# Kernel tuning notes

Measured on AMD Instinct MI355X. Metric: run time of the kernel, lower is better.

The kernel has to match this reference:

```python
import jax, jax.numpy as jnp
import numpy as np

N_NODES = 50000
N_EDGES = 800000
DIM = 128  # in_dim == out_dim (required by the original module's math)
BN_EPS = 1e-5


def setup_inputs() -> dict:
    key = jax.random.key(0)
    ks = jax.random.split(key, 12)
    d = DIM
    s = 1.0 / np.sqrt(d)
    x = jax.random.normal(ks[0], (N_NODES, d), dtype=jnp.float32)
    edge_index = jax.random.randint(ks[1], (2, N_EDGES), 0, N_NODES, dtype=jnp.int64)
    # message_fn: Linear(in_dim, out_dim)
    W_msg = jax.random.uniform(ks[2], (d, d), jnp.float32, -s, s)
    b_msg = jax.random.uniform(ks[3], (d,), jnp.float32, -s, s)
    # attention: Linear(2*in_dim, 1)
    sa = 1.0 / np.sqrt(2 * d)
    W_att = jax.random.uniform(ks[4], (2 * d, 1), jnp.float32, -sa, sa)
    b_att = jax.random.uniform(ks[5], (1,), jnp.float32, -sa, sa)
    # GRUCell(out_dim, out_dim): weight_ih [3d, d], weight_hh [3d, d]
    W_ih = jax.random.uniform(ks[6], (3 * d, d), jnp.float32, -s, s)
    b_ih = jax.random.uniform(ks[7], (3 * d,), jnp.float32, -s, s)
    W_hh = jax.random.uniform(ks[8], (3 * d, d), jnp.float32, -s, s)
    b_hh = jax.random.uniform(ks[9], (3 * d,), jnp.float32, -s, s)
    # BatchNorm1d(out_dim)
    gamma = jnp.ones((d,), jnp.float32)
    beta = jnp.zeros((d,), jnp.float32)
    return {"x": x, "edge_index": edge_index, "W_msg": W_msg, "b_msg": b_msg,
            "W_att": W_att, "b_att": b_att, "W_ih": W_ih, "b_ih": b_ih,
            "W_hh": W_hh, "b_hh": b_hh, "gamma": gamma, "beta": beta}


def reference(x, edge_index, W_msg, b_msg, W_att, b_att, W_ih, b_ih, W_hh, b_hh, gamma, beta):
    num_nodes, d = x.shape
    src = edge_index[0]
    dst = edge_index[1]
    xs = x[src]            # [E, d] gather
    xd = x[dst]            # [E, d] gather
    # sigmoid(cat([xs, xd]) @ W_att + b_att) without materializing the concat
    att = jax.nn.sigmoid(xs @ W_att[:d] + xd @ W_att[d:] + b_att)  # [E, 1]
    messages = (xs @ W_msg + b_msg) * att                          # [E, d]
    aggregated = jax.ops.segment_sum(messages, dst, num_segments=num_nodes)  # scatter-add
    # GRUCell(aggregated, x)
    gi = aggregated @ W_ih.T + b_ih   # [N, 3d]
    gh = x @ W_hh.T + b_hh            # [N, 3d]
    i_r, i_z, i_n = jnp.split(gi, 3, axis=1)
    h_r, h_z, h_n = jnp.split(gh, 3, axis=1)
    r = jax.nn.sigmoid(i_r + h_r)
    z = jax.nn.sigmoid(i_z + h_z)
    n = jnp.tanh(i_n + r * h_n)
    h_new = (1.0 - z) * n + z * x
    # dropout is identity in eval mode; BatchNorm1d in training mode (batch stats, biased var)
    mean = jnp.mean(h_new, axis=0)
    var = jnp.var(h_new, axis=0)
    return gamma * (h_new - mean) * jax.lax.rsqrt(var + BN_EPS) + beta
```

## Files before the change

### kernel.cpp

```cpp
#include <hip/hip_runtime.h>
#include <hip/hip_bf16.h>
#include <hip/hip_fp16.h>

#define DIM 128
#define SWS 136
typedef __hip_bfloat16 bf16;
typedef __attribute__((ext_vector_type(8))) short bf16x8;
typedef __attribute__((ext_vector_type(4))) float f32x4;

__device__ __forceinline__ float b2f(bf16 v) { return __bfloat162float(v); }
__device__ __forceinline__ bf16  f2b(float v) { return __float2bfloat16(v); }

template<bool F32>
__device__ __forceinline__ float ldf(const void* p, size_t i) {
    if (F32) return ((const float*)p)[i];
    else     return b2f(((const bf16*)p)[i]);
}
template<bool F32>
__device__ __forceinline__ void stf(void* p, size_t i, float v) {
    if (F32) ((float*)p)[i] = v;
    else     ((bf16*)p)[i] = f2b(v);
}

__device__ __forceinline__ bf16x8 pack8_f32(const float* p) {
    bf16x8 r;
#pragma unroll
    for (int i = 0; i < 8; ++i) { bf16 t = f2b(p[i]); r[i] = *(const short*)&t; }
    return r;
}
template<bool F32>
__device__ __forceinline__ bf16x8 load_frag(const void* base, size_t off) {
    if (F32) return pack8_f32((const float*)base + off);
    else     return *(const bf16x8*)((const unsigned short*)base + off);
}

__device__ __forceinline__ float bflo(unsigned int m) { return __uint_as_float(m << 16); }
__device__ __forceinline__ float bfhi(unsigned int m) { return __uint_as_float(m & 0xFFFF0000u); }

__device__ __forceinline__ float sigmoidf_fast(float v) { return 1.0f / (1.0f + __expf(-v)); }
__device__ __forceinline__ float tanhf_fast(float t) {
    float e2 = __expf(2.0f * t);
    return 1.0f - 2.0f / (e2 + 1.0f);
}

__global__ void detect_kernel(const void* __restrict__ ei, const void* __restrict__ gamma,
                              int n_nodes, int* __restrict__ flags)
{
    if (blockIdx.x == 0 && threadIdx.x == 0) {
        const long long* e64 = (const long long*)ei;
        int ok = 1;
        for (int i = 0; i < 16; ++i) {
            long long v = e64[i];
            if (v < 0 || v >= (long long)n_nodes) ok = 0;
        }
        flags[0] = ok;
        const float* g = (const float*)gamma;
        flags[1] = (fabsf(g[0] - 1.0f) < 1e-6f && fabsf(g[1] - 1.0f) < 1e-6f) ? 1 : 0;
    }
}

__device__ void atomic_add_bf16(bf16* addr, float val)
{
    unsigned int* base = (unsigned int*)((size_t)addr & ~(size_t)3);
    bool hi = ((size_t)addr & 2) != 0;
    unsigned int old = *base, assumed;
    do {
        assumed = old;
        unsigned short cur = hi ? (unsigned short)(assumed >> 16) : (unsigned short)(assumed & 0xFFFF);
        bf16 cb = *(bf16*)&cur;
        bf16 nb = f2b(b2f(cb) + val);
        unsigned short ns = *(unsigned short*)&nb;
        unsigned int newv = hi ? ((assumed & 0x0000FFFFu) | ((unsigned int)ns << 16))
                               : ((assumed & 0xFFFF0000u) | (unsigned int)ns);
        old = atomicCAS(base, assumed, newv);
    } while (old != assumed);
}

#define NW (144 * 128)
#define NI (384 * 128)
#define PREPN (NW + 2 * NI)
__global__ __launch_bounds__(256) void prep_hist_kernel(
    const void* __restrict__ W_msg, const void* __restrict__ W_att,
    const void* __restrict__ W_ih, const void* __restrict__ W_hh,
    unsigned short* __restrict__ wbuf,
    const void* __restrict__ ei, int* __restrict__ deg, int n_edges,
    int prep_blocks, const int* __restrict__ flags)
{
    if ((int)blockIdx.x < prep_blocks) {
        bool f32 = flags[1] != 0;
        int i = blockIdx.x * blockDim.x + threadIdx.x;
        if (i >= PREPN) return;
        float v;
        if (i < NW) {
            int j = i >> 7, k = i & 127;
            if (j < 128)       v = f32 ? ((const float*)W_msg)[k * 128 + j] : b2f(((const bf16*)W_msg)[k * 128 + j]);
            else if (j == 128) v = f32 ? ((const float*)W_att)[k]           : b2f(((const bf16*)W_att)[k]);
            else if (j == 129) v = f32 ? ((const float*)W_att)[128 + k]     : b2f(((const bf16*)W_att)[128 + k]);
            else               v = 0.0f;
        } else if (i < NW + NI) {
            int t = i - NW;
            v = f32 ? ((const float*)W_ih)[t] : b2f(((const bf16*)W_ih)[t]);
        } else {
            int t = i - NW - NI;
            v = f32 ? ((const float*)W_hh)[t] : b2f(((const bf16*)W_hh)[t]);
        }
        bf16 b = f2b(v);
        wbuf[i] = *(unsigned short*)&b;
    } else {
        int i = ((int)blockIdx.x - prep_blocks) * blockDim.x + threadIdx.x;
        if (i >= n_edges) return;
        int t = flags[0] ? (int)((const long long*)ei)[n_edges + i] : ((const int*)ei)[n_edges + i];
        atomicAdd(&deg[t], 1);
    }
}

template<bool F32>
__device__ void node_mfma_body(unsigned short* __restrict__ sw,
                               const void* __restrict__ x, const unsigned short* __restrict__ Wnode,
                               const void* __restrict__ b_msg, unsigned short* __restrict__ Mb,
                               float* __restrict__ a_src, float* __restrict__ a_dst, int n_nodes)
{
    int wave = threadIdx.x >> 6, lane = threadIdx.x & 63;
    int m0 = (blockIdx.x * 4 + wave) * 16;
    int mrow = lane & 15, quad = lane >> 4;
    bool active = (m0 < n_nodes);
    int mnode = active ? (m0 + mrow < n_nodes ? m0 + mrow : n_nodes - 1) : 0;

    {
        int t = threadIdx.x;
#pragma unroll
        for (int i = 0; i < 9; ++i) {
            int v = t + i * 256;
            if (v < 2304) {
                int row = v >> 4, col = (v & 15) * 8;
                *(bf16x8*)(sw + row * SWS + col) = *(const bf16x8*)(Wnode + row * DIM + col);
            }
        }
    }

    bf16x8 a[4];
#pragma unroll
    for (int kq = 0; kq < 4; ++kq)
        a[kq] = load_frag<F32>(x, (size_t)mnode * DIM + kq * 32 + quad * 8);

    __syncthreads();

#pragma unroll
    for (int jt = 0; jt < 9; ++jt) {
        const unsigned short* wr = sw + (jt * 16 + mrow) * SWS + quad * 8;
        bf16x8 B[4];
#pragma unroll
        for (int kq = 0; kq < 4; ++kq)
            B[kq] = *(const bf16x8*)(wr + kq * 32);
        f32x4 acc = {0, 0, 0, 0};
#pragma unroll
        for (int kq = 0; kq < 4; ++kq)
            acc = __builtin_amdgcn_mfma_f32_16x16x32_bf16(a[kq], B[kq], acc, 0, 0, 0);
        if (!active) continue;
        if (jt < 8) {
            int jcol = jt * 16 + mrow;
            float bm = ldf<F32>(b_msg, jcol);
#pragma unroll
            for (int rg = 0; rg < 4; ++rg) {
                int node = m0 + quad * 4 + rg;
                if (node < n_nodes) {
                    bf16 bb = f2b(acc[rg] + bm);
                    Mb[(size_t)node * DIM + jcol] = *(unsigned short*)&bb;
                }
            }
        } else if (mrow < 2) {
#pragma unroll
            for (int rg = 0; rg < 4; ++rg) {
                int node = m0 + quad * 4 + rg;
                if (node < n_nodes) {
                    if (mrow == 0) a_src[node] = acc[rg];
                    else           a_dst[node] = acc[rg];
                }
            }
        }
    }
}

__global__ __launch_bounds__(256) void node_mfma_kernel(
    const void* x, const unsigned short* Wnode, const void* b_msg,
    unsigned short* Mb, float* a_src, float* a_dst, int n_nodes, const int* __restrict__ flags)
{
    __shared__ unsigned short sw[144 * SWS];
    if (flags[1]) node_mfma_body<true>(sw, x, Wnode, b_msg, Mb, a_src, a_dst, n_nodes);
    else          node_mfma_body<false>(sw, x, Wnode, b_msg, Mb, a_src, a_dst, n_nodes);
}

__global__ __launch_bounds__(256) void partial_sum_kernel(
    const int* __restrict__ deg, int* __restrict__ partials, int n_nodes)
{
    __shared__ int s[256];
    int t = threadIdx.x;
    int i = blockIdx.x * 256 + t;
    s[t] = (i < n_nodes) ? deg[i] : 0;
    __syncthreads();
    for (int off = 128; off > 0; off >>= 1) {
        if (t < off) s[t] += s[t + off];
        __syncthreads();
    }
    if (t == 0) partials[blockIdx.x] = s[0];
}

__global__ __launch_bounds__(256) void scan_write_kernel(
    const int* __restrict__ deg, const int* __restrict__ partials,
    int* __restrict__ row_start, int* __restrict__ fill, int n_nodes, int n_edges,
    int nblocks)
{
    __shared__ int s[256];
    __shared__ int sp[256];
    int t = threadIdx.x;
    int i = blockIdx.x * 256 + t;
    int v = (i < n_nodes) ? deg[i] : 0;
    int pv = (t < nblocks) ? partials[t] : 0;
    s[t] = v;
    sp[t] = pv;
    __syncthreads();
    for (int off = 1; off < 256; off <<= 1) {
        int u  = (t >= off) ? s[t - off]  : 0;
        int up = (t >= off) ? sp[t - off] : 0;
        __syncthreads();
        s[t] += u;
        sp[t] += up;
        __syncthreads();
    }
    int block_off = (blockIdx.x == 0) ? 0 : sp[blockIdx.x - 1];
    int excl = s[t] - v + block_off;
    if (i < n_nodes) { row_start[i] = excl; fill[i] = excl; }
    if (blockIdx.x == 0 && t == 0) row_start[n_nodes] = n_edges;
}

template<bool PACK4>
__global__ __launch_bounds__(256) void scatter_kernel(
    const void* __restrict__ ei, const float* __restrict__ a_src, const float* __restrict__ a_dst,
    const void* __restrict__ b_att, int* __restrict__ fill,
    void* __restrict__ edata, const int* __restrict__ flags, int n_edges)
{
    int i = blockIdx.x * blockDim.x + threadIdx.x;
    if (i >= n_edges) return;
    int s, t;
    if (flags[0]) {
        const long long* p = (const long long*)ei;
        s = (int)p[i]; t = (int)p[n_edges + i];
    } else {
        const int* p = (const int*)ei;
        s = p[i]; t = p[n_edges + i];
    }
    float battv = flags[1] ? ((const float*)b_att)[0] : b2f(((const bf16*)b_att)[0]);
    int pos = atomicAdd(&fill[t], 1);
    float logit = a_src[s] + a_dst[t] + battv;
    float att = 1.0f / (1.0f + __expf(-logit));
    if (PACK4) {
        __half h = __float2half(att);
        unsigned int rec = ((unsigned int)s << 16) | (unsigned int)(*(unsigned short*)&h);
        ((unsigned int*)edata)[pos] = rec;
    } else {
        uint2 rec;
        rec.x = (unsigned int)s;
        rec.y = __float_as_uint(att);
        ((uint2*)edata)[pos] = rec;
    }
}

template<bool PACK4>
__global__ __launch_bounds__(256) void aggregate_kernel(
    const unsigned short* __restrict__ Mb, const int* __restrict__ row_start,
    const void* __restrict__ edata, unsigned short* __restrict__ aggb, int n_nodes)
{
    int w = (int)((blockIdx.x * (unsigned)blockDim.x + threadIdx.x) >> 6);
    int lane = threadIdx.x & 63;
    if (w >= n_nodes) return;
    int beg = row_start[w], end = row_start[w + 1];
    float acc0 = 0.0f, acc1 = 0.0f;
    const unsigned int* e4 = (const unsigned int*)edata;
    const uint2* e8 = (const uint2*)edata;
    int e = beg;
    for (; e + 4 <= end; e += 4) {
        unsigned int src[4]; float wt[4];
#pragma unroll
        for (int k = 0; k < 4; ++k) {
            if (PACK4) {
                unsigned int r = e4[e + k];
                src[k] = r >> 16;
                unsigned short hb = (unsigned short)(r & 0xFFFF);
                wt[k] = __half2float(*(__half*)&hb);
            } else {
                uint2 r = e8[e + k];
                src[k] = r.x;
                wt[k] = __uint_as_float(r.y);
            }
        }
        unsigned int m0 = *(const unsigned int*)(Mb + ((size_t)src[0] << 7) + lane * 2);
        unsigned int m1 = *(const unsigned int*)(Mb + ((size_t)src[1] << 7) + lane * 2);
        unsigned int m2 = *(const unsigned int*)(Mb + ((size_t)src[2] << 7) + lane * 2);
        unsigned int m3 = *(const unsigned int*)(Mb + ((size_t)src[3] << 7) + lane * 2);
        acc0 += wt[0] * bflo(m0) + wt[1] * bflo(m1) + wt[2] * bflo(m2) + wt[3] * bflo(m3);
        acc1 += wt[0] * bfhi(m0) + wt[1] * bfhi(m1) + wt[2] * bfhi(m2) + wt[3] * bfhi(m3);
    }
    for (; e < end; ++e) {
        unsigned int sidx; float a;
        if (PACK4) {
            unsigned int r = e4[e];
            sidx = r >> 16;
            unsigned short hb = (unsigned short)(r & 0xFFFF);
            a = __half2float(*(__half*)&hb);
        } else {
            uint2 r = e8[e];
            sidx = r.x;
            a = __uint_as_float(r.y);
        }
        unsigned int m = *(const unsigned int*)(Mb + ((size_t)sidx << 7) + lane * 2);
        acc0 += a * bflo(m);
        acc1 += a * bfhi(m);
    }
    bf16 r0 = f2b(acc0), r1 = f2b(acc1);
    unsigned int packed = (unsigned int)(*(unsigned short*)&r0) |
                          ((unsigned int)(*(unsigned short*)&r1) << 16);
    *(unsigned int*)(aggb + ((size_t)w << 7) + lane * 2) = packed;
}

template<bool F32>
__device__ void gru_mfma_body(unsigned short* __restrict__ sw,
                              const void* __restrict__ x, const unsigned short* __restrict__ aggb,
                              const unsigned short* __restrict__ Wih, const unsigned short* __restrict__ Whh,
                              const void* __restrict__ b_ih, const void* __restrict__ b_hh,
                              void* __restrict__ h_out, int n_nodes)
{
    const int BUF = 96 * SWS;
    int wave = threadIdx.x >> 6, lane = threadIdx.x & 63;
    int m0 = (blockIdx.x * 4 + wave) * 16;
    int mrow = lane & 15, quad = lane >> 4;
    bool active = (m0 < n_nodes);
    int mnode = active ? (m0 + mrow < n_nodes ? m0 + mrow : n_nodes - 1) : 0;

    int t = threadIdx.x;
    int srow[6], scol[6];
    const unsigned short* sbase[6];
#pragma unroll
    for (int i = 0; i < 6; ++i) {
        int v = t + i * 256;
        int row = v >> 4;
        scol[i] = (v & 15) * 8;
        srow[i] = row;
        int g = row >> 4;
        sbase[i] = ((g < 3) ? Wih : Whh) + (size_t)((g % 3) * 128 + (row & 15)) * DIM;
    }

    bf16x8 a_ag[4], a_x[4];
#pragma unroll
    for (int kq = 0; kq < 4; ++kq) {
        a_ag[kq] = *(const bf16x8*)(aggb + (size_t)mnode * DIM + kq * 32 + quad * 8);
        a_x[kq]  = load_frag<F32>(x, (size_t)mnode * DIM + kq * 32 + quad * 8);
    }

#pragma unroll
    for (int i = 0; i < 6; ++i) {
        bf16x8 d = *(const bf16x8*)(sbase[i] + scol[i]);
        *(bf16x8*)(sw + srow[i] * SWS + scol[i]) = d;
    }
    __syncthreads();

    float hprev[4];

    for (int jt = 0; jt < 8; ++jt) {
        unsigned short* cur = sw + (jt & 1) * BUF;
        unsigned short* nxt = sw + ((jt + 1) & 1) * BUF;

        bf16x8 pf[6];
        if (jt < 7) {
#pragma unroll
            for (int i = 0; i < 6; ++i)
                pf[i] = *(const bf16x8*)(sbase[i] + (size_t)(jt + 1) * 16 * DIM + scol[i]);
        }

        f32x4 acc_ir = {0,0,0,0}, acc_iz = {0,0,0,0}, acc_in = {0,0,0,0};
        f32x4 acc_hr = {0,0,0,0}, acc_hz = {0,0,0,0}, acc_hn = {0,0,0,0};

#pragma unroll
        for (int half = 0; half < 2; ++half) {
            bf16x8 B[12];
#pragma unroll
            for (int kq = 0; kq < 2; ++kq) {
                int k = half * 2 + kq;
                int boff = mrow * SWS + k * 32 + quad * 8;
#pragma unroll
                for (int g = 0; g < 6; ++g)
                    B[kq * 6 + g] = *(const bf16x8*)(cur + g * (16 * SWS) + boff);
            }
#pragma unroll
            for (int kq = 0; kq < 2; ++kq) {
                int k = half * 2 + kq;
                acc_ir = __builtin_amdgcn_mfma_f32_16x16x32_bf16(a_ag[k], B[kq * 6 + 0], acc_ir, 0, 0, 0);
                acc_iz = __builtin_amdgcn_mfma_f32_16x16x32_bf16(a_ag[k], B[kq * 6 + 1], acc_iz, 0, 0, 0);
                acc_in = __builtin_amdgcn_mfma_f32_16x16x32_bf16(a_ag[k], B[kq * 6 + 2], acc_in, 0, 0, 0);
                acc_hr = __builtin_amdgcn_mfma_f32_16x16x32_bf16(a_x[k],  B[kq * 6 + 3], acc_hr, 0, 0, 0);
                acc_hz = __builtin_amdgcn_mfma_f32_16x16x32_bf16(a_x[k],  B[kq * 6 + 4], acc_hz, 0, 0, 0);
                acc_hn = __builtin_amdgcn_mfma_f32_16x16x32_bf16(a_x[k],  B[kq * 6 + 5], acc_hn, 0, 0, 0);
            }
        }

        if (jt < 7) {
#pragma unroll
            for (int i = 0; i < 6; ++i)
                *(bf16x8*)(nxt + srow[i] * SWS + scol[i]) = pf[i];
        }

        if (active) {
            int jcol = jt * 16 + mrow;
            float xsv[4];
#pragma unroll
            for (int rg = 0; rg < 4; ++rg) {
                int node = m0 + quad * 4 + rg;
                int nclamp = node < n_nodes ? node : (n_nodes - 1);
                xsv[rg] = ldf<F32>(x, (size_t)nclamp * DIM + jcol);
            }
            float bir = ldf<F32>(b_ih, jcol), biz = ldf<F32>(b_ih, 128 + jcol), bin_ = ldf<F32>(b_ih, 256 + jcol);
            float bhr = ldf<F32>(b_hh, jcol), bhz = ldf<F32>(b_hh, 128 + jcol), bhn  = ldf<F32>(b_hh, 256 + jcol);
            float hcur[4];
#pragma unroll
            for (int rg = 0; rg < 4; ++rg) {
                float gir = acc_ir[rg] + bir, giz = acc_iz[rg] + biz, gin = acc_in[rg] + bin_;
                float ghr = acc_hr[rg] + bhr, ghz = acc_hz[rg] + bhz, ghn = acc_hn[rg] + bhn;
                float r = sigmoidf_fast(gir + ghr);
                float z = sigmoidf_fast(giz + ghz);
                float nn = tanhf_fast(gin + r * ghn);
                hcur[rg] = (1.0f - z) * nn + z * xsv[rg];
            }
            if ((jt & 1) == 0) {
#pragma unroll
                for (int rg = 0; rg < 4; ++rg) hprev[rg] = hcur[rg];
            } else {
#pragma unroll
                for (int rg = 0; rg < 4; ++rg) {
                    int node = m0 + quad * 4 + rg;
                    if (node >= n_nodes) continue;
                    stf<F32>(h_out, (size_t)node * DIM + jcol - 16, hprev[rg]);
                    stf<F32>(h_out, (size_t)node * DIM + jcol,      hcur[rg]);
                }
            }
        }
        __syncthreads();
    }
}

__global__ __launch_bounds__(256) void gru_mfma_kernel(
    const void* x, const unsigned short* aggb, const unsigned short* Wih, const unsigned short* Whh,
    const void* b_ih, const void* b_hh, void* h_out, int n_nodes, const int* __restrict__ flags)
{
    __shared__ unsigned short sw[2 * 96 * SWS];
    if (flags[1]) gru_mfma_body<true>(sw, x, aggb, Wih, Whh, b_ih, b_hh, h_out, n_nodes);
    else          gru_mfma_body<false>(sw, x, aggb, Wih, Whh, b_ih, b_hh, h_out, n_nodes);
}

template<bool F32>
__device__ void node_pre_body(const void* __restrict__ x, const void* __restrict__ W_msg,
                              const void* __restrict__ b_msg, const void* __restrict__ W_att,
                              void* __restrict__ M, float* __restrict__ a_src,
                              float* __restrict__ a_dst)
{
    int n = blockIdx.x;
    int j = threadIdx.x;
    __shared__ float xs[DIM], r1[DIM], r2[DIM];
    float xv = ldf<F32>(x, (size_t)n * DIM + j);
    xs[j] = xv;
    r1[j] = xv * ldf<F32>(W_att, j);
    r2[j] = xv * ldf<F32>(W_att, DIM + j);
    __syncthreads();
    float acc = ldf<F32>(b_msg, j);
#pragma unroll 8
    for (int k = 0; k < DIM; ++k)
        acc += xs[k] * ldf<F32>(W_msg, (size_t)k * DIM + j);
    stf<F32>(M, (size_t)n * DIM + j, acc);
    for (int s = 64; s > 0; s >>= 1) {
        __syncthreads();
        if (j < s) { r1[j] += r1[j + s]; r2[j] += r2[j + s]; }
    }
    if (j == 0) { a_src[n] = r1[0]; a_dst[n] = r2[0]; }
}

__global__ __launch_bounds__(128) void node_pre_kernel(
    const void* x, const void* W_msg, const void* b_msg, const void* W_att,
    void* M, float* a_src, float* a_dst, const int* __restrict__ flags)
{
    if (flags[1]) node_pre_body<true>(x, W_msg, b_msg, W_att, M, a_src, a_dst);
    else          node_pre_body<false>(x, W_msg, b_msg, W_att, M, a_src, a_dst);
}

template<bool F32, bool AGGF32>
__device__ void edge_body(const void* __restrict__ ei, const void* __restrict__ M,
                          const float* __restrict__ a_src, const float* __restrict__ a_dst,
                          const void* __restrict__ b_att, void* __restrict__ agg,
                          int idx64, int n_edges)
{
    int e = (int)((blockIdx.x * (unsigned)blockDim.x + threadIdx.x) >> 6);
    int lane = threadIdx.x & 63;
    if (e >= n_edges) return;
    int s, t;
    if (idx64) {
        const long long* p = (const long long*)ei;
        s = (int)p[e]; t = (int)p[n_edges + e];
    } else {
        const int* p = (const int*)ei;
        s = p[e]; t = p[n_edges + e];
    }
    float logit = a_src[s] + a_dst[t] + ldf<F32>(b_att, 0);
    float attv = 1.0f / (1.0f + __expf(-logit));
    float m0 = ldf<F32>(M, (size_t)s * DIM + lane) * attv;
    float m1 = ldf<F32>(M, (size_t)s * DIM + 64 + lane) * attv;
    if (AGGF32) {
        float* a = (float*)agg;
        atomicAdd(&a[(size_t)t * DIM + lane], m0);
        atomicAdd(&a[(size_t)t * DIM + 64 + lane], m1);
    } else {
        bf16* a = (bf16*)agg;
        atomic_add_bf16(&a[(size_t)t * DIM + lane], m0);
        atomic_add_bf16(&a[(size_t)t * DIM + 64 + lane], m1);
    }
}

template<bool AGGF32>
__global__ __launch_bounds__(256) void edge_kernel(
    const void* ei, const void* M, const float* a_src, const float* a_dst,
    const void* b_att, void* agg, const int* __restrict__ flags, int n_edges)
{
    if (flags[1]) edge_body<true, AGGF32>(ei, M, a_src, a_dst, b_att, agg, flags[0], n_edges);
    else          edge_body<false, AGGF32>(ei, M, a_src, a_dst, b_att, agg, flags[0], n_edges);
}

#define NPB 8
template<bool F32, bool AGGF32>
__device__ void gru_body(const void* __restrict__ x, const void* __restrict__ agg,
                         const void* __restrict__ W_ih, const void* __restrict__ b_ih,
                         const void* __restrict__ W_hh, const void* __restrict__ b_hh,
                         void* __restrict__ h_new, int n_nodes)
{
    int node0 = blockIdx.x * NPB;
    int j = threadIdx.x;
    __shared__ float ag[NPB][DIM];
    __shared__ float xv[NPB][DIM];
    __shared__ float gi[NPB][3 * DIM];
    __shared__ float gh[NPB][3 * DIM];
    for (int i = j; i < NPB * DIM; i += 384) {
        int nn = i >> 7, d = i & 127;
        int node = node0 + nn;
        if (node < n_nodes) {
            ag[nn][d] = AGGF32 ? ((const float*)agg)[(size_t)node * DIM + d]
                               : b2f(((const bf16*)agg)[(size_t)node * DIM + d]);
            xv[nn][d] = ldf<F32>(x, (size_t)node * DIM + d);
        } else { ag[nn][d] = 0.0f; xv[nn][d] = 0.0f; }
    }
    __syncthreads();
    {
        float acc_i[NPB], acc_h[NPB];
        float bi = ldf<F32>(b_ih, j);
        float bh = ldf<F32>(b_hh, j);
#pragma unroll
        for (int m = 0; m < NPB; ++m) { acc_i[m] = bi; acc_h[m] = bh; }
#pragma unroll 4
        for (int k = 0; k < DIM; ++k) {
            float wik = ldf<F32>(W_ih, (size_t)j * DIM + k);
            float whk = ldf<F32>(W_hh, (size_t)j * DIM + k);
#pragma unroll
            for (int m = 0; m < NPB; ++m) {
                acc_i[m] += ag[m][k] * wik;
                acc_h[m] += xv[m][k] * whk;
            }
        }
#pragma unroll
        for (int m = 0; m < NPB; ++m) { gi[m][j] = acc_i[m]; gh[m][j] = acc_h[m]; }
    }
    __syncthreads();
    for (int i = j; i < NPB * DIM; i += 384) {
        int nn = i >> 7, d = i & 127;
        int node = node0 + nn;
        if (node >= n_nodes) continue;
        float r = 1.0f / (1.0f + __expf(-(gi[nn][d] + gh[nn][d])));
        float z = 1.0f / (1.0f + __expf(-(gi[nn][DIM + d] + gh[nn][DIM + d])));
        float nv = tanhf(gi[nn][2 * DIM + d] + r * gh[nn][2 * DIM + d]);
        float h = (1.0f - z) * nv + z * xv[nn][d];
        stf<F32>(h_new, (size_t)node * DIM + d, h);
    }
}

template<bool AGGF32>
__global__ __launch_bounds__(384) void gru_kernel(
    const void* x, const void* agg, const void* W_ih, const void* b_ih,
    const void* W_hh, const void* b_hh, void* h_new, int n_nodes,
    const int* __restrict__ flags)
{
    if (flags[1]) gru_body<true, AGGF32>(x, agg, W_ih, b_ih, W_hh, b_hh, h_new, n_nodes);
    else          gru_body<false, AGGF32>(x, agg, W_ih, b_ih, W_hh, b_hh, h_new, n_nodes);
}

template<bool F32>
__device__ void bn_stats_body(const void* __restrict__ h, float* __restrict__ sums, int n_nodes)
{
    __shared__ float s1[256], s2[256];
    int tid = threadIdx.x;
    int d = tid & 127, half = tid >> 7;
    float acc = 0.0f, accsq = 0.0f;
    for (int node = blockIdx.x * 2 + half; node < n_nodes; node += gridDim.x * 2) {
        float v = ldf<F32>(h, (size_t)node * DIM + d);
        acc += v; accsq += v * v;
    }
    s1[tid] = acc; s2[tid] = accsq;
    __syncthreads();
    if (tid < 128) {
        atomicAdd(&sums[d], s1[tid] + s1[tid + 128]);
        atomicAdd(&sums[DIM + d], s2[tid] + s2[tid + 128]);
    }
}

__global__ __launch_bounds__(256) void bn_stats_kernel(
    const void* h, float* sums, int n_nodes, const int* __restrict__ flags)
{
    if (flags[1]) bn_stats_body<true>(h, sums, n_nodes);
    else          bn_stats_body<false>(h, sums, n_nodes);
}

template<bool F32>
__device__ void bn_norm_body(void* __restrict__ h, const float* __restrict__ sums,
                             const void* __restrict__ gamma, const void* __restrict__ beta,
                             int n_nodes)
{
    int idx = blockIdx.x * blockDim.x + threadIdx.x;
    int total = n_nodes * DIM;
    if (idx >= total) return;
    int d = idx & 127;
    float inv_n = 1.0f / (float)n_nodes;
    float mean = sums[d] * inv_n;
    float var = sums[DIM + d] * inv_n - mean * mean;
    float inv = rsqrtf(var + 1e-5f);
    float v = ldf<F32>(h, idx);
    stf<F32>(h, idx, (v - mean) * inv * ldf<F32>(gamma, d) + ldf<F32>(beta, d));
}

__global__ __launch_bounds__(256) void bn_norm_kernel(
    void* h, const float* sums, const void* gamma, const void* beta,
    int n_nodes, const int* __restrict__ flags)
{
    if (flags[1]) bn_norm_body<true>(h, sums, gamma, beta, n_nodes);
    else          bn_norm_body<false>(h, sums, gamma, beta, n_nodes);
}

extern "C" void kernel_launch(void* const* d_in, const int* in_sizes, int n_in,
                              void* d_out, int out_size, void* d_ws, size_t ws_size,
                              hipStream_t stream)
{
    const void* x     = d_in[0];
    const void* ei    = d_in[1];
    const void* W_msg = d_in[2];
    const void* b_msg = d_in[3];
    const void* W_att = d_in[4];
    const void* b_att = d_in[5];
    const void* W_ih  = d_in[6];
    const void* b_ih  = d_in[7];
    const void* W_hh  = d_in[8];
    const void* b_hh  = d_in[9];
    const void* gamma = d_in[10];
    const void* beta  = d_in[11];

    int n_nodes = in_sizes[0] / DIM;
    int n_edges = in_sizes[1] / 2;
    size_t nd = (size_t)n_nodes * DIM;

    int*   flags = (int*)d_ws;
    float* sums  = (float*)(flags + 64);
    float* a_src = sums + 256;
    float* a_dst = a_src + n_nodes;
    unsigned short* aggb = (unsigned short*)(a_dst + n_nodes);
    unsigned short* wbuf = aggb + nd;
    int* deg       = (int*)(wbuf + NW + 2 * NI);
    int* row_start = deg + n_nodes;
    int* fill      = row_start + n_nodes + 1;
    int* partials  = fill + n_nodes;
    char* ep = (char*)(partials + 256);
    ep = (char*)(((size_t)ep + 15) & ~(size_t)15);
    void* edata = (void*)ep;
    size_t need_main = (size_t)(ep + (size_t)n_edges * 8 - (char*)d_ws);

    hipMemsetAsync(sums, 0, 256 * sizeof(float), stream);
    detect_kernel<<<1, 64, 0, stream>>>(ei, gamma, n_nodes, flags);

    int total = n_nodes * DIM;
    int norm_blocks = (total + 255) / 256;
    int tiles = (n_nodes + 15) / 16;
    int tblocks4 = (tiles + 3) / 4;
    int eblocks = (n_edges + 255) / 256;
    int sblocks = (n_nodes + 255) / 256;
    int prep_blocks = (PREPN + 255) / 256;
    bool pack4 = (n_nodes <= 65536);

    if (ws_size >= need_main && sblocks <= 256) {
        hipMemsetAsync(deg, 0, (size_t)n_nodes * sizeof(int), stream);
        prep_hist_kernel<<<prep_blocks + eblocks, 256, 0, stream>>>(
            W_msg, W_att, W_ih, W_hh, wbuf, ei, deg, n_edges, prep_blocks, flags);
        unsigned short* Mb = (unsigned short*)d_out;
        node_mfma_kernel<<<tblocks4, 256, 0, stream>>>(
            x, wbuf, b_msg, Mb, a_src, a_dst, n_nodes, flags);
        partial_sum_kernel<<<sblocks, 256, 0, stream>>>(deg, partials, n_nodes);
        scan_write_kernel<<<sblocks, 256, 0, stream>>>(deg, partials, row_start, fill, n_nodes, n_edges, sblocks);
        if (pack4) {
            scatter_kernel<true><<<eblocks, 256, 0, stream>>>(
                ei, a_src, a_dst, b_att, fill, edata, flags, n_edges);
            aggregate_kernel<true><<<(n_nodes + 3) / 4, 256, 0, stream>>>(
                Mb, row_start, edata, aggb, n_nodes);
        } else {
            scatter_kernel<false><<<eblocks, 256, 0, stream>>>(
                ei, a_src, a_dst, b_att, fill, edata, flags, n_edges);
            aggregate_kernel<false><<<(n_nodes + 3) / 4, 256, 0, stream>>>(
                Mb, row_start, edata, aggb, n_nodes);
        }
        gru_mfma_kernel<<<tblocks4, 256, 0, stream>>>(
            x, aggb, wbuf + NW, wbuf + NW + NI, b_ih, b_hh, d_out, n_nodes, flags);
    } else {
        char* big = (char*)(a_dst + n_nodes);
        size_t small_bytes = (size_t)(big - (char*)d_ws);
        int edge_blocks = (int)(((size_t)n_edges * 64 + 255) / 256);
        if (ws_size >= small_bytes + nd * sizeof(float)) {
            float* agg = (float*)big;
            hipMemsetAsync(agg, 0, nd * sizeof(float), stream);
            node_pre_kernel<<<n_nodes, 128, 0, stream>>>(x, W_msg, b_msg, W_att, d_out, a_src, a_dst, flags);
            edge_kernel<true><<<edge_blocks, 256, 0, stream>>>(ei, d_out, a_src, a_dst, b_att, agg, flags, n_edges);
            gru_kernel<true><<<(n_nodes + NPB - 1) / NPB, 384, 0, stream>>>(x, agg, W_ih, b_ih, W_hh, b_hh, d_out, n_nodes, flags);
        } else {
            bf16* agg = (bf16*)big;
            hipMemsetAsync(agg, 0, nd * sizeof(bf16), stream);
            node_pre_kernel<<<n_nodes, 128, 0, stream>>>(x, W_msg, b_msg, W_att, d_out, a_src, a_dst, flags);
            edge_kernel<false><<<edge_blocks, 256, 0, stream>>>(ei, d_out, a_src, a_dst, b_att, agg, flags, n_edges);
            gru_kernel<false><<<(n_nodes + NPB - 1) / NPB, 384, 0, stream>>>(x, agg, W_ih, b_ih, W_hh, b_hh, d_out, n_nodes, flags);
        }
    }

    bn_stats_kernel<<<512, 256, 0, stream>>>(d_out, sums, n_nodes, flags);
    bn_norm_kernel<<<norm_blocks, 256, 0, stream>>>(d_out, sums, gamma, beta, n_nodes, flags);
}
```

Baseline: 301.5 us.

## Two-pass bucketed edge scatter and fold memsets into detect kernel

Replaces the single random scatter of edge records into CSR order with a two-pass scheme. The first pass bins each chunk of 2048 edges by 256-node destination bucket, using shared-memory counters and one global atomic per bucket. The second pass scatters from these partially sorted records, so writes and fill atomics land close together. The deg and sums memsets are folded into a grid-wide detect kernel to remove separate memset launches. In exchange it adds a temp buffer of n_edges*8 bytes, an extra kernel launch and an extra full pass over the edge records.

```diff
diff --git a/kernel.cpp b/kernel.cpp
--- a/kernel.cpp
+++ b/kernel.cpp
@@ -43,9 +43,13 @@
     return 1.0f - 2.0f / (e2 + 1.0f);
 }
 
-__global__ void detect_kernel(const void* __restrict__ ei, const void* __restrict__ gamma,
-                              int n_nodes, int* __restrict__ flags)
-{
+__global__ __launch_bounds__(256) void detect_kernel(
+    const void* __restrict__ ei, const void* __restrict__ gamma,
+    int n_nodes, int* __restrict__ flags, int* __restrict__ deg, float* __restrict__ sums)
+{
+    for (int i = blockIdx.x * 256 + threadIdx.x; i < n_nodes; i += gridDim.x * 256)
+        deg[i] = 0;
+    if (blockIdx.x == 0) sums[threadIdx.x] = 0.0f;
     if (blockIdx.x == 0 && threadIdx.x == 0) {
         const long long* e64 = (const long long*)ei;
         int ok = 1;
@@ -207,8 +211,8 @@
 
 __global__ __launch_bounds__(256) void scan_write_kernel(
     const int* __restrict__ deg, const int* __restrict__ partials,
-    int* __restrict__ row_start, int* __restrict__ fill, int n_nodes, int n_edges,
-    int nblocks)
+    int* __restrict__ row_start, int* __restrict__ fill, int* __restrict__ bfill,
+    int n_nodes, int n_edges, int nblocks)
 {
     __shared__ int s[256];
     __shared__ int sp[256];
@@ -229,15 +233,86 @@
     }
     int block_off = (blockIdx.x == 0) ? 0 : sp[blockIdx.x - 1];
     int excl = s[t] - v + block_off;
-    if (i < n_nodes) { row_start[i] = excl; fill[i] = excl; }
+    if (i < n_nodes) {
+        row_start[i] = excl;
+        fill[i] = excl;
+        if ((i & 255) == 0) bfill[i >> 8] = excl;
+    }
     if (blockIdx.x == 0 && t == 0) row_start[n_nodes] = n_edges;
 }
 
-template<bool PACK4>
-__global__ __launch_bounds__(256) void scatter_kernel(
+#define CH 2048
+__global__ __launch_bounds__(256) void bucket_scatter_kernel(
+    const void* __restrict__ ei, const float* __restrict__ a_src, const float* __restrict__ a_dst,
+    const void* __restrict__ b_att, int* __restrict__ bfill,
+    uint2* __restrict__ tmp, const int* __restrict__ flags, int n_edges)
+{
+    __shared__ int cnt[256];
+    __shared__ int base[256];
+    int tid = threadIdx.x;
+    int c0 = blockIdx.x * CH;
+    float battv = flags[1] ? ((const float*)b_att)[0] : b2f(((const bf16*)b_att)[0]);
+    bool i64 = flags[0] != 0;
+
+    cnt[tid] = 0;
+    __syncthreads();
+
+    int myb[8]; int mydst[8]; unsigned int myrec[8];
+#pragma unroll
+    for (int k = 0; k < 8; ++k) {
+        int i = c0 + k * 256 + tid;
+        if (i < n_edges) {
+            int s, t;
+            if (i64) {
+                const long long* p = (const long long*)ei;
+                s = (int)p[i]; t = (int)p[n_edges + i];
+            } else {
+                const int* p = (const int*)ei;
+                s = p[i]; t = p[n_edges + i];
+            }
+            float att = sigmoidf_fast(a_src[s] + a_dst[t] + battv);
+            __half h = __float2half(att);
+            myb[k] = t >> 8;
+            mydst[k] = t;
+            myrec[k] = ((unsigned int)s << 16) | (unsigned int)(*(unsigned short*)&h);
+            atomicAdd(&cnt[t >> 8], 1);
+        } else myb[k] = -1;
+    }
+    __syncthreads();
+
+    int c = cnt[tid];
+    if (c > 0) base[tid] = atomicAdd(&bfill[tid], c);
+    __syncthreads();
+    cnt[tid] = 0;
+    __syncthreads();
+
+#pragma unroll
+    for (int k = 0; k < 8; ++k) {
+        if (myb[k] >= 0) {
+            int loc = atomicAdd(&cnt[myb[k]], 1);
+            uint2 rec;
+            rec.x = (unsigned int)mydst[k];
+            rec.y = myrec[k];
+            tmp[base[myb[k]] + loc] = rec;
+        }
+    }
+}
+
+__global__ __launch_bounds__(256) void final_scatter_kernel(
+    const uint2* __restrict__ tmp, int* __restrict__ fill,
+    unsigned int* __restrict__ edata, int n_edges)
+{
+    int i = blockIdx.x * blockDim.x + threadIdx.x;
+    if (i >= n_edges) return;
+    uint2 r = tmp[i];
+    int pos = atomicAdd(&fill[r.x], 1);
+    edata[pos] = r.y;
+}
+
+__global__ __launch_bounds__(256) void scatter8_kernel(
     const void* __restrict__ ei, const float* __restrict__ a_src, const float* __restrict__ a_dst,
     const void* __restrict__ b_att, int* __restrict__ fill,
-    void* __restrict__ edata, const int* __restrict__ flags, int n_edges)
+    uint2* __restrict__ edata, const int* __restrict__ flags, int n_edges)
 {
     int i = blockIdx.x * blockDim.x + threadIdx.x;
     if (i >= n_edges) return;
@@ -251,18 +326,11 @@
     }
     float battv = flags[1] ? ((const float*)b_att)[0] : b2f(((const bf16*)b_att)[0]);
     int pos = atomicAdd(&fill[t], 1);
-    float logit = a_src[s] + a_dst[t] + battv;
-    float att = 1.0f / (1.0f + __expf(-logit));
-    if (PACK4) {
-        __half h = __float2half(att);
-        unsigned int rec = ((unsigned int)s << 16) | (unsigned int)(*(unsigned short*)&h);
-        ((unsigned int*)edata)[pos] = rec;
-    } else {
-        uint2 rec;
-        rec.x = (unsigned int)s;
-        rec.y = __float_as_uint(att);
-        ((uint2*)edata)[pos] = rec;
-    }
+    float att = sigmoidf_fast(a_src[s] + a_dst[t] + battv);
+    uint2 rec;
+    rec.x = (unsigned int)s;
+    rec.y = __float_as_uint(att);
+    edata[pos] = rec;
 }
 
 template<bool PACK4>
@@ -677,13 +745,12 @@
     int* row_start = deg + n_nodes;
     int* fill      = row_start + n_nodes + 1;
     int* partials  = fill + n_nodes;
-    char* ep = (char*)(partials + 256);
+    int* bfill     = partials + 256;
+    char* ep = (char*)(bfill + 256);
     ep = (char*)(((size_t)ep + 15) & ~(size_t)15);
     void* edata = (void*)ep;
-    size_t need_main = (size_t)(ep + (size_t)n_edges * 8 - (char*)d_ws);
-
-    hipMemsetAsync(sums, 0, 256 * sizeof(float), stream);
-    detect_kernel<<<1, 64, 0, stream>>>(ei, gamma, n_nodes, flags);
+    uint2* tmp = (uint2*)(ep + (size_t)n_edges * 8);
+    size_t need_main = (size_t)((char*)(tmp + n_edges) - (char*)d_ws);
 
     int total = n_nodes * DIM;
     int norm_blocks = (total + 255) / 256;
@@ -692,31 +759,38 @@
     int eblocks = (n_edges + 255) / 256;
     int sblocks = (n_nodes + 255) / 256;
     int prep_blocks = (PREPN + 255) / 256;
+    int chunk_blocks = (n_edges + CH - 1) / CH;
     bool pack4 = (n_nodes <= 65536);
 
     if (ws_size >= need_main && sblocks <= 256) {
-        hipMemsetAsync(deg, 0, (size_t)n_nodes * sizeof(int), stream);
+        detect_kernel<<<sblocks, 256, 0, stream>>>(ei, gamma, n_nodes, flags, deg, sums);
         prep_hist_kernel<<<prep_blocks + eblocks, 256, 0, stream>>>(
             W_msg, W_att, W_ih, W_hh, wbuf, ei, deg, n_edges, prep_blocks, flags);
         unsigned short* Mb = (unsigned short*)d_out;
         node_mfma_kernel<<<tblocks4, 256, 0, stream>>>(
             x, wbuf, b_msg, Mb, a_src, a_dst, n_nodes, flags);
         partial_sum_kernel<<<sblocks, 256, 0, stream>>>(deg, partials, n_nodes);
-        scan_write_kernel<<<sblocks, 256, 0, stream>>>(deg, partials, row_start, fill, n_nodes, n_edges, sblocks);
+        scan_write_kernel<<<sblocks, 256, 0, stream>>>(
+            deg, partials, row_start, fill, bfill, n_nodes, n_edges, sblocks);
         if (pack4) {
-            scatter_kernel<true><<<eblocks, 256, 0, stream>>>(
-                ei, a_src, a_dst, b_att, fill, edata, flags, n_edges);
+            bucket_scatter_kernel<<<chunk_blocks, 256, 0, stream>>>(
+                ei, a_src, a_dst, b_att, bfill, tmp, flags, n_edges);
+            final_scatter_kernel<<<eblocks, 256, 0, stream>>>(
+                tmp, fill, (unsigned int*)edata, n_edges);
             aggregate_kernel<true><<<(n_nodes + 3) / 4, 256, 0, stream>>>(
                 Mb, row_start, edata, aggb, n_nodes);
         } else {
-            scatter_kernel<false><<<eblocks, 256, 0, stream>>>(
-                ei, a_src, a_dst, b_att, fill, edata, flags, n_edges);
+            scatter8_kernel<<<eblocks, 256, 0, stream>>>(
+                ei, a_src, a_dst, b_att, fill, (uint2*)edata, flags, n_edges);
             aggregate_kernel<false><<<(n_nodes + 3) / 4, 256, 0, stream>>>(
                 Mb, row_start, edata, aggb, n_nodes);
         }
         gru_mfma_kernel<<<tblocks4, 256, 0, stream>>>(
             x, aggb, wbuf + NW, wbuf + NW + NI, b_ih, b_hh, d_out, n_nodes, flags);
+        bn_stats_kernel<<<512, 256, 0, stream>>>(d_out, sums, n_nodes, flags);
+        bn_norm_kernel<<<norm_blocks, 256, 0, stream>>>(d_out, sums, gamma, beta, n_nodes, flags);
     } else {
+        detect_kernel<<<sblocks, 256, 0, stream>>>(ei, gamma, n_nodes, flags, deg, sums);
         char* big = (char*)(a_dst + n_nodes);
         size_t small_bytes = (size_t)(big - (char*)d_ws);
         int edge_blocks = (int)(((size_t)n_edges * 64 + 255) / 256);
@@ -733,8 +807,7 @@
             edge_kernel<false><<<edge_blocks, 256, 0, stream>>>(ei, d_out, a_src, a_dst, b_att, agg, flags, n_edges);
             gru_kernel<false><<<(n_nodes + NPB - 1) / NPB, 384, 0, stream>>>(x, agg, W_ih, b_ih, W_hh, b_hh, d_out, n_nodes, flags);
         }
-    }
-
-    bn_stats_kernel<<<512, 256, 0, stream>>>(d_out, sums, n_nodes, flags);
-    bn_norm_kernel<<<norm_blocks, 256, 0, stream>>>(d_out, sums, gamma, beta, n_nodes, flags);
-}
+        bn_stats_kernel<<<512, 256, 0, stream>>>(d_out, sums, n_nodes, flags);
+        bn_norm_kernel<<<norm_blocks, 256, 0, stream>>>(d_out, sums, gamma, beta, n_nodes, flags);
+    }
+}
```

Measured after the change: 298.3 us. About the same (-1.1%).
